# Kernel optimization log

Hardware: AMD Instinct MI355X
Metric: run time of the kernel (lower is better)

## Reference

```python
import jax, jax.numpy as jnp
import numpy as np

D_MODEL = 768
NUM_HEADS = 12
SEQ_LEN = 4096
BATCH = 1


def setup_inputs() -> dict:
    key = jax.random.key(0)
    k1, k2, k3, k4 = jax.random.split(key, 4)
    x = jax.random.normal(k1, (BATCH, SEQ_LEN, D_MODEL), dtype=jnp.float32)
    # nn.Linear(d_model, 3*d_model, bias=False): store as [d_model, 3*d_model] so h = x @ w_qkv
    w_qkv = jax.random.normal(k2, (D_MODEL, 3 * D_MODEL), dtype=jnp.float32) * (1.0 / np.sqrt(D_MODEL))
    w_proj = jax.random.normal(k3, (D_MODEL, D_MODEL), dtype=jnp.float32) * (1.0 / np.sqrt(D_MODEL))
    b_proj = jax.random.normal(k4, (D_MODEL,), dtype=jnp.float32) * 0.01
    return {"x": x, "w_qkv": w_qkv, "w_proj": w_proj, "b_proj": b_proj}


def reference(x, w_qkv, w_proj, b_proj):
    n, t, c = x.shape
    H = NUM_HEADS
    dh = c // H
    # fused QKV projection: [n, t, 3c] -> per head contiguous [q|k|v] chunks of dh
    h = (x @ w_qkv).reshape(n, t, H, 3, dh)
    q = h[..., 0, :]  # [n, t, H, dh]
    k = h[..., 1, :]
    v = h[..., 2, :]
    scale = 1.0 / np.sqrt(dh)
    # full TxT score matrix, as in the hand-rolled torch module
    scores = jnp.einsum('nqhd,nkhd->nhqk', q, k) * scale  # [n, H, t, t]
    causal = jnp.tril(jnp.ones((t, t), dtype=bool))  # tril buffer
    scores = jnp.where(causal, scores, jnp.finfo(scores.dtype).min)
    att = jax.nn.softmax(scores, axis=-1)
    out = jnp.einsum('nhqk,nkhd->nqhd', att, v).reshape(n, t, c)
    return out @ w_proj + b_proj
```

## Files before the change

### kernel.cpp

```cpp
#include <hip/hip_runtime.h>

#define T_SEQ 4096
#define DM    768
#define NH    12
#define DH    64
#define NC    2304

using half8  = __attribute__((ext_vector_type(8))) _Float16;
using half4v = __attribute__((ext_vector_type(4))) _Float16;
using f32x4  = __attribute__((ext_vector_type(4))) float;
using f32x16 = __attribute__((ext_vector_type(16))) float;
typedef unsigned int u32;

union H8 { half8 v; u32 u[4]; };

__device__ __forceinline__ u32 pkrtz_u32(float a, float b) {
    return __builtin_bit_cast(u32, __builtin_amdgcn_cvt_pkrtz(a, b));
}
__device__ __forceinline__ float asf(u32 x) { return __builtin_bit_cast(float, x); }
__device__ __forceinline__ u32 asu(float x) { return __builtin_bit_cast(u32, x); }

__device__ __forceinline__ void async_copy16(void* lds, const void* g) {
    __builtin_amdgcn_global_load_lds(
        (const __attribute__((address_space(1))) u32*)g,
        (__attribute__((address_space(3))) u32*)lds, 16, 0, 0);
}

__global__ __launch_bounds__(256)
void convert_x_kernel(const float* __restrict__ x, _Float16* __restrict__ xh) {
    const size_t i = ((size_t)blockIdx.x * 256 + threadIdx.x) * 8;
    float4 a = *(const float4*)(x + i);
    float4 b = *(const float4*)(x + i + 4);
    half8 o = { (_Float16)a.x, (_Float16)a.y, (_Float16)a.z, (_Float16)a.w,
                (_Float16)b.x, (_Float16)b.y, (_Float16)b.z, (_Float16)b.w };
    *(half8*)(xh + i) = o;
}

__global__ __launch_bounds__(256)
void transpose_convert_kernel(const float* __restrict__ src,
                              _Float16* __restrict__ dst, int R, int C) {
    __shared__ _Float16 tile[64][72];
    const int tid = threadIdx.x;
    const int tc0 = blockIdx.x * 64;
    const int tr0 = blockIdx.y * 64;
    const int r = tid >> 2, c4 = (tid & 3) * 16;
    const float* sp = src + (size_t)(tr0 + r) * C + tc0 + c4;
    #pragma unroll
    for (int j = 0; j < 16; j += 4) {
        float4 t4 = *(const float4*)(sp + j);
        tile[r][c4 + j + 0] = (_Float16)t4.x;
        tile[r][c4 + j + 1] = (_Float16)t4.y;
        tile[r][c4 + j + 2] = (_Float16)t4.z;
        tile[r][c4 + j + 3] = (_Float16)t4.w;
    }
    __syncthreads();
    const int c = tid >> 2, r4 = (tid & 3) * 16;
    half8 o0, o1;
    #pragma unroll
    for (int j = 0; j < 8; ++j) o0[j] = tile[r4 + j][c];
    #pragma unroll
    for (int j = 0; j < 8; ++j) o1[j] = tile[r4 + 8 + j][c];
    _Float16* dp = dst + (size_t)(tc0 + c) * R + tr0 + r4;
    *(half8*)(dp) = o0;
    *(half8*)(dp + 8) = o1;
}

__global__ __launch_bounds__(256, 2)
void qkv_mfma_kernel(const _Float16* __restrict__ A,
                     const _Float16* __restrict__ Bt,
                     _Float16* __restrict__ q, _Float16* __restrict__ k,
                     _Float16* __restrict__ v) {
    __shared__ _Float16 Alds[128 * 64];
    __shared__ _Float16 Blds[128 * 64];
    const int tid  = threadIdx.x;
    const int lane = tid & 63;
    const int w    = tid >> 6;
    const int wr = w >> 1, wc = w & 1;
    const int lrow = lane >> 4, lcol = lane & 15;

    const int bid  = blockIdx.x;
    const int virt = (bid & 7) * 72 + (bid >> 3);
    const int cbn  = virt % 18, rbn = virt / 18;

    const _Float16* Ag = A  + (size_t)rbn * 128 * DM;
    const _Float16* Bg = Bt + (size_t)cbn * 128 * DM;

    int srow[4], scol[4];
    #pragma unroll
    for (int i = 0; i < 4; ++i) {
        const int idx = i * 256 + tid;
        srow[i] = idx >> 3;
        scol[i] = ((idx & 7) ^ (srow[i] & 7)) * 8;
    }

    f32x4 acc[4][4];
    #pragma unroll
    for (int mf = 0; mf < 4; ++mf)
        #pragma unroll
        for (int nf = 0; nf < 4; ++nf) acc[mf][nf] = (f32x4){0.f, 0.f, 0.f, 0.f};

    for (int kt = 0; kt < DM / 64; ++kt) {
        const int k0 = kt * 64;
        __syncthreads();
        #pragma unroll
        for (int i = 0; i < 4; ++i) {
            async_copy16((char*)Alds + (i * 256 + w * 64) * 16,
                         Ag + (size_t)srow[i] * DM + k0 + scol[i]);
            async_copy16((char*)Blds + (i * 256 + w * 64) * 16,
                         Bg + (size_t)srow[i] * DM + k0 + scol[i]);
        }
        __syncthreads();
        #pragma unroll
        for (int kh = 0; kh < 2; ++kh) {
            half8 af[4], bf[4];
            const int ag = kh * 4 + lrow;
            #pragma unroll
            for (int f = 0; f < 4; ++f) {
                const int ar = wr * 64 + f * 16 + lcol;
                af[f] = *(const half8*)((const char*)Alds +
                          ar * 128 + ((ag ^ (ar & 7)) << 4));
                const int br = wc * 64 + f * 16 + lcol;
                bf[f] = *(const half8*)((const char*)Blds +
                          br * 128 + ((ag ^ (br & 7)) << 4));
            }
            #pragma unroll
            for (int mf = 0; mf < 4; ++mf)
                #pragma unroll
                for (int nf = 0; nf < 4; ++nf)
                    acc[mf][nf] = __builtin_amdgcn_mfma_f32_16x16x32_f16(
                        af[mf], bf[nf], acc[mf][nf], 0, 0, 0);
        }
    }

    #pragma unroll
    for (int nf = 0; nf < 4; ++nf) {
        const int n = cbn * 128 + wc * 64 + nf * 16 + lcol;
        const int head  = n / 192;
        const int which = (n >> 6) % 3;
        const int d = n & 63;
        _Float16* dst = (which == 0) ? q : (which == 1) ? k : v;
        const float sc = (which == 0) ? 0.18033688011112042f : 1.0f;
        dst += (size_t)head * T_SEQ * DH + d;
        #pragma unroll
        for (int mf = 0; mf < 4; ++mf) {
            const int t0 = rbn * 128 + wr * 64 + mf * 16 + lrow * 4;
            #pragma unroll
            for (int r = 0; r < 4; ++r)
                dst[(size_t)(t0 + r) * DH] = (_Float16)(acc[mf][nf][r] * sc);
        }
    }
}

__global__ __launch_bounds__(256, 2)
void proj_mfma_kernel(const _Float16* __restrict__ A,
                      const _Float16* __restrict__ Bt,
                      const float* __restrict__ bias, float* __restrict__ out) {
    __shared__ _Float16 Alds[128 * 64];
    __shared__ _Float16 Blds[128 * 64];
    const int tid  = threadIdx.x;
    const int lane = tid & 63;
    const int w    = tid >> 6;
    const int wr = w >> 1, wc = w & 1;
    const int lrow = lane >> 4, lcol = lane & 15;

    const int bid  = blockIdx.x;
    const int virt = (bid & 7) * 24 + (bid >> 3);
    const int cbn  = virt % 6, rbn = virt / 6;

    const _Float16* Ag = A  + (size_t)rbn * 128 * DM;
    const _Float16* Bg = Bt + (size_t)cbn * 128 * DM;

    int srow[4], scol[4];
    #pragma unroll
    for (int i = 0; i < 4; ++i) {
        const int idx = i * 256 + tid;
        srow[i] = idx >> 3;
        scol[i] = ((idx & 7) ^ (srow[i] & 7)) * 8;
    }

    f32x4 acc[4][4];
    #pragma unroll
    for (int mf = 0; mf < 4; ++mf)
        #pragma unroll
        for (int nf = 0; nf < 4; ++nf) acc[mf][nf] = (f32x4){0.f, 0.f, 0.f, 0.f};

    for (int kt = 0; kt < DM / 64; ++kt) {
        const int k0 = kt * 64;
        __syncthreads();
        #pragma unroll
        for (int i = 0; i < 4; ++i) {
            async_copy16((char*)Alds + (i * 256 + w * 64) * 16,
                         Ag + (size_t)srow[i] * DM + k0 + scol[i]);
            async_copy16((char*)Blds + (i * 256 + w * 64) * 16,
                         Bg + (size_t)srow[i] * DM + k0 + scol[i]);
        }
        __syncthreads();
        #pragma unroll
        for (int kh = 0; kh < 2; ++kh) {
            half8 af[4], bf[4];
            const int ag = kh * 4 + lrow;
            #pragma unroll
            for (int f = 0; f < 4; ++f) {
                const int ar = wr * 64 + f * 16 + lcol;
                af[f] = *(const half8*)((const char*)Alds +
                          ar * 128 + ((ag ^ (ar & 7)) << 4));
                const int br = wc * 64 + f * 16 + lcol;
                bf[f] = *(const half8*)((const char*)Blds +
                          br * 128 + ((ag ^ (br & 7)) << 4));
            }
            #pragma unroll
            for (int mf = 0; mf < 4; ++mf)
                #pragma unroll
                for (int nf = 0; nf < 4; ++nf)
                    acc[mf][nf] = __builtin_amdgcn_mfma_f32_16x16x32_f16(
                        af[mf], bf[nf], acc[mf][nf], 0, 0, 0);
        }
    }

    #pragma unroll
    for (int nf = 0; nf < 4; ++nf) {
        const int n = cbn * 128 + wc * 64 + nf * 16 + lcol;
        const float b = bias[n];
        #pragma unroll
        for (int mf = 0; mf < 4; ++mf) {
            const int t0 = rbn * 128 + wr * 64 + mf * 16 + lrow * 4;
            #pragma unroll
            for (int r = 0; r < 4; ++r)
                out[(size_t)(t0 + r) * DM + n] = acc[mf][nf][r] + b;
        }
    }
}

__global__ __launch_bounds__(256)
void vt_kernel(const _Float16* __restrict__ v, _Float16* __restrict__ vt) {
    __shared__ _Float16 tile[64][65];
    const int tid = threadIdx.x;
    const int tb = blockIdx.x, h = blockIdx.y;
    const int r = tid >> 2, c0 = (tid & 3) * 16;
    const _Float16* src = v + ((size_t)h * T_SEQ + tb * 64 + r) * 64 + c0;
    half8 a0 = *(const half8*)(src);
    half8 a1 = *(const half8*)(src + 8);
    #pragma unroll
    for (int j = 0; j < 8; ++j) tile[r][c0 + j] = a0[j];
    #pragma unroll
    for (int j = 0; j < 8; ++j) tile[r][c0 + 8 + j] = a1[j];
    __syncthreads();
    const int d = tid >> 2, t0 = (tid & 3) * 16;
    half8 o0, o1;
    #pragma unroll
    for (int j = 0; j < 8; ++j) o0[j] = tile[t0 + j][d];
    #pragma unroll
    for (int j = 0; j < 8; ++j) o1[j] = tile[t0 + 8 + j][d];
    _Float16* dst = vt + ((size_t)h * 64 + d) * T_SEQ + tb * 64 + t0;
    *(half8*)(dst) = o0;
    *(half8*)(dst + 8) = o1;
}

__global__ __launch_bounds__(256)
void attn_tile_kernel(const _Float16* __restrict__ qg,
                      const _Float16* __restrict__ kg,
                      const _Float16* __restrict__ vtg,
                      _Float16* __restrict__ pO,
                      float* __restrict__ pml) {
    __shared__ _Float16 Kl[2][4096];
    __shared__ _Float16 Vl[2][4096];

    const int tid  = threadIdx.x;
    const int lane = tid & 63;
    const int w    = tid >> 6;
    const int l31  = lane & 31;
    const int hi   = lane >> 5;

    const int b = blockIdx.x;
    const int h = b % NH;
    const int i = 79 - b / NH;
    int j, seg;
    if (i < 8)       { j = i;                  seg = 0; }
    else if (i < 24) { const int t = i - 8;    j = 8  + (t >> 1); seg = t & 1; }
    else if (i < 48) { const int t = i - 24;   j = 16 + t / 3;    seg = t % 3; }
    else             { const int t = i - 48;   j = 24 + (t >> 2); seg = t & 3; }

    const int cw      = 4 * j + w;
    const int q       = cw * 32 + l31;
    const int niter_w = 2 * j + 1 + (w >> 1);
    const int tS      = seg * 16;
    const int tEndBlk = min(tS + 16, 2 * j + 2);
    const int tEndW   = min(tS + 16, niter_w);

    const _Float16* Qh = qg  + ((size_t)h * T_SEQ + q) * DH;
    const _Float16* Kh = kg  + (size_t)h * T_SEQ * DH;
    const _Float16* Vh = vtg + (size_t)h * DH * T_SEQ;

    half8 qf[4];
    #pragma unroll
    for (int ks = 0; ks < 4; ++ks)
        qf[ks] = *(const half8*)(Qh + ks * 16 + hi * 8);

    f32x16 o0v = {}, o1v = {};
    float l = 0.f;

    const int g0 = tid, g1 = tid + 256;
    const int r0 = g0 >> 3, s0 = ((g0 & 7) ^ (r0 & 7)) * 8;
    const int r1 = g1 >> 3, s1 = ((g1 & 7) ^ (r1 & 7)) * 8;

    auto stage = [&](int p, int kvb) {
        async_copy16((char*)Kl[p] + g0 * 16, Kh + (size_t)(kvb + r0) * DH + s0);
        async_copy16((char*)Kl[p] + g1 * 16, Kh + (size_t)(kvb + r1) * DH + s1);
        async_copy16((char*)Vl[p] + g0 * 16, Vh + (size_t)r0 * T_SEQ + kvb + s0);
        async_copy16((char*)Vl[p] + g1 * 16, Vh + (size_t)r1 * T_SEQ + kvb + s1);
    };

    stage(0, tS * 64);
    for (int it = tS; it < tEndBlk; ++it) {
        const int p = (it - tS) & 1;
        __syncthreads();
        if (it + 1 < tEndBlk) stage(p ^ 1, (it + 1) * 64);
        if (it >= tEndW) continue;

        const int kvb = it * 64;
        const char* Kb = (const char*)Kl[p];
        const char* Vb = (const char*)Vl[p];
        const int sw7 = l31 & 7;

        half8 kfA[4], kfB[4];
        #pragma unroll
        for (int ks = 0; ks < 4; ++ks) {
            const int gsl = (ks * 2 + hi) ^ sw7;
            kfA[ks] = *(const half8*)(Kb + l31 * 128 + (gsl << 4));
            kfB[ks] = *(const half8*)(Kb + (32 + l31) * 128 + (gsl << 4));
        }
        half8 vf[2][2][2];
        #pragma unroll
        for (int t = 0; t < 2; ++t)
            #pragma unroll
            for (int dt = 0; dt < 2; ++dt)
                #pragma unroll
                for (int ks2 = 0; ks2 < 2; ++ks2) {
                    const int gsl = (t * 4 + ks2 * 2 + hi) ^ sw7;
                    vf[t][dt][ks2] = *(const half8*)(Vb +
                        (dt * 32 + l31) * 128 + (gsl << 4));
                }

        f32x16 sA, sB;
        #pragma unroll
        for (int r = 0; r < 16; ++r) { sA[r] = -8.0f; sB[r] = -8.0f; }
        __builtin_amdgcn_s_setprio(1);
        #pragma unroll
        for (int ks = 0; ks < 4; ++ks) {
            sA = __builtin_amdgcn_mfma_f32_32x32x16_f16(kfA[ks], qf[ks], sA, 0, 0, 0);
            sB = __builtin_amdgcn_mfma_f32_32x32x16_f16(kfB[ks], qf[ks], sB, 0, 0, 0);
        }
        __builtin_amdgcn_s_setprio(0);

        if (it == niter_w - 1) {
            #pragma unroll
            for (int r = 0; r < 16; ++r) {
                const int off = (r & 3) + 8 * (r >> 2) + 4 * hi;
                if (kvb + off > q)      sA[r] = -1e30f;
                if (kvb + 32 + off > q) sB[r] = -1e30f;
            }
        }

        #pragma unroll
        for (int r = 0; r < 16; ++r) sA[r] = __builtin_amdgcn_exp2f(sA[r]);
        #pragma unroll
        for (int r = 0; r < 16; ++r) sB[r] = __builtin_amdgcn_exp2f(sB[r]);
        float s8[8];
        #pragma unroll
        for (int r = 0; r < 8; ++r)
            s8[r] = (sA[r] + sA[r + 8]) + (sB[r] + sB[r + 8]);
        float rsum = ((s8[0] + s8[4]) + (s8[1] + s8[5])) +
                     ((s8[2] + s8[6]) + (s8[3] + s8[7]));
        {
            auto r = __builtin_amdgcn_permlane32_swap(asu(rsum), asu(rsum), false, false);
            rsum = asf(r[0]) + asf(r[1]);
        }
        l += rsum;

        H8 pfA[2], pfB[2];
        #pragma unroll
        for (int ks2 = 0; ks2 < 2; ++ks2) {
            {
                const u32 a0 = pkrtz_u32(sA[8*ks2+0], sA[8*ks2+1]);
                const u32 a1 = pkrtz_u32(sA[8*ks2+2], sA[8*ks2+3]);
                const u32 b0 = pkrtz_u32(sA[8*ks2+4], sA[8*ks2+5]);
                const u32 b1 = pkrtz_u32(sA[8*ks2+6], sA[8*ks2+7]);
                auto r0v = __builtin_amdgcn_permlane32_swap(a0, b0, false, false);
                auto r1v = __builtin_amdgcn_permlane32_swap(a1, b1, false, false);
                pfA[ks2].u[0] = r0v[0];
                pfA[ks2].u[1] = r1v[0];
                pfA[ks2].u[2] = r0v[1];
                pfA[ks2].u[3] = r1v[1];
            }
            {
                const u32 a0 = pkrtz_u32(sB[8*ks2+0], sB[8*ks2+1]);
                const u32 a1 = pkrtz_u32(sB[8*ks2+2], sB[8*ks2+3]);
                const u32 b0 = pkrtz_u32(sB[8*ks2+4], sB[8*ks2+5]);
                const u32 b1 = pkrtz_u32(sB[8*ks2+6], sB[8*ks2+7]);
                auto r0v = __builtin_amdgcn_permlane32_swap(a0, b0, false, false);
                auto r1v = __builtin_amdgcn_permlane32_swap(a1, b1, false, false);
                pfB[ks2].u[0] = r0v[0];
                pfB[ks2].u[1] = r1v[0];
                pfB[ks2].u[2] = r0v[1];
                pfB[ks2].u[3] = r1v[1];
            }
        }

        __builtin_amdgcn_s_setprio(1);
        #pragma unroll
        for (int ks2 = 0; ks2 < 2; ++ks2) {
            o0v = __builtin_amdgcn_mfma_f32_32x32x16_f16(vf[0][0][ks2], pfA[ks2].v, o0v, 0, 0, 0);
            o1v = __builtin_amdgcn_mfma_f32_32x32x16_f16(vf[0][1][ks2], pfA[ks2].v, o1v, 0, 0, 0);
            o0v = __builtin_amdgcn_mfma_f32_32x32x16_f16(vf[1][0][ks2], pfB[ks2].v, o0v, 0, 0, 0);
            o1v = __builtin_amdgcn_mfma_f32_32x32x16_f16(vf[1][1][ks2], pfB[ks2].v, o1v, 0, 0, 0);
        }
        __builtin_amdgcn_s_setprio(0);
    }

    const int hc = h * 128 + cw;
    const float inv = (l > 0.f) ? 1.0f / l : 0.f;
    _Float16* op = pO + ((size_t)(seg * 1536 + hc) * 32 + l31) * 64 + 4 * hi;
    #pragma unroll
    for (int g = 0; g < 4; ++g) {
        half4v w0 = { (_Float16)(o0v[4*g+0] * inv), (_Float16)(o0v[4*g+1] * inv),
                      (_Float16)(o0v[4*g+2] * inv), (_Float16)(o0v[4*g+3] * inv) };
        half4v w1 = { (_Float16)(o1v[4*g+0] * inv), (_Float16)(o1v[4*g+1] * inv),
                      (_Float16)(o1v[4*g+2] * inv), (_Float16)(o1v[4*g+3] * inv) };
        *(half4v*)(op + 8 * g)      = w0;
        *(half4v*)(op + 32 + 8 * g) = w1;
    }
    if (hi == 0) {
        float* mp = pml + ((size_t)(seg * 1536 + hc) * 32 + l31) * 2;
        mp[0] = 0.0f;
        mp[1] = l;
    }
}

__global__ __launch_bounds__(256)
void attn_combine_kernel(const _Float16* __restrict__ pO,
                         const float* __restrict__ pml,
                         _Float16* __restrict__ att) {
    const int row = blockIdx.x * 256 + threadIdx.x;
    const int q5 = row & 31;
    const int hc = row >> 5;
    const int c  = hc & 127;
    const int h  = hc >> 7;
    const int nseg = 1 + (c >= 32) + (c >= 64) + (c >= 96);

    float mm[4], ll[4];
    float M = -1e30f;
    #pragma unroll
    for (int s = 0; s < 4; ++s) {
        const bool on = s < nseg;
        const float* mp = pml + ((size_t)(s * 1536 + hc) * 32 + q5) * 2;
        mm[s] = on ? mp[0] : -1e30f;
        ll[s] = on ? mp[1] : 0.f;
        M = fmaxf(M, mm[s]);
    }
    float wgt[4];
    float L = 0.f;
    #pragma unroll
    for (int s = 0; s < 4; ++s) {
        wgt[s] = ll[s] * __builtin_amdgcn_exp2f(mm[s] - M);
        L += wgt[s];
    }
    const float invL = 1.0f / L;
    #pragma unroll
    for (int s = 0; s < 4; ++s) wgt[s] *= invL;

    float acc[64];
    #pragma unroll
    for (int d = 0; d < 64; ++d) acc[d] = 0.f;
    #pragma unroll
    for (int s = 0; s < 4; ++s) {
        if (s >= nseg) break;
        const _Float16* src = pO + ((size_t)(s * 1536 + hc) * 32 + q5) * 64;
        const float wsc = wgt[s];
        #pragma unroll
        for (int g = 0; g < 8; ++g) {
            half8 v = *(const half8*)(src + g * 8);
            #pragma unroll
            for (int jj = 0; jj < 8; ++jj)
                acc[g * 8 + jj] += wsc * (float)v[jj];
        }
    }
    _Float16* dst = att + (size_t)(c * 32 + q5) * DM + h * DH;
    #pragma unroll
    for (int g = 0; g < 8; ++g) {
        half8 o;
        #pragma unroll
        for (int jj = 0; jj < 8; ++jj) o[jj] = (_Float16)acc[g * 8 + jj];
        *(half8*)(dst + g * 8) = o;
    }
}

extern "C" void kernel_launch(void* const* d_in, const int* in_sizes, int n_in,
                              void* d_out, int out_size, void* d_ws, size_t ws_size,
                              hipStream_t stream) {
    const float* x      = (const float*)d_in[0];
    const float* w_qkv  = (const float*)d_in[1];
    const float* w_proj = (const float*)d_in[2];
    const float* b_proj = (const float*)d_in[3];
    float* out = (float*)d_out;

    _Float16* wsb = (_Float16*)d_ws;
    const size_t XS = (size_t)T_SEQ * DM;
    const size_t HS = (size_t)NH * T_SEQ * DH;
    _Float16* xh     = wsb;
    _Float16* wqkvT  = xh + XS;
    _Float16* wprojT = wqkvT + (size_t)NC * DM;
    _Float16* q      = wprojT + (size_t)DM * DM;
    _Float16* k      = q + HS;
    _Float16* v      = k + HS;
    _Float16* vt     = v + HS;
    _Float16* att    = vt + HS;
    _Float16* pO     = att + XS;
    float*    pml    = (float*)(pO + (size_t)4 * 1536 * 32 * 64);

    convert_x_kernel<<<dim3(1536), 256, 0, stream>>>(x, xh);
    transpose_convert_kernel<<<dim3(36, 12), 256, 0, stream>>>(w_qkv, wqkvT, DM, NC);
    transpose_convert_kernel<<<dim3(12, 12), 256, 0, stream>>>(w_proj, wprojT, DM, DM);
    qkv_mfma_kernel<<<dim3(576), 256, 0, stream>>>(xh, wqkvT, q, k, v);
    vt_kernel<<<dim3(64, NH), 256, 0, stream>>>(v, vt);
    attn_tile_kernel<<<dim3(960), 256, 0, stream>>>(q, k, vt, pO, pml);
    attn_combine_kernel<<<dim3(192), 256, 0, stream>>>(pO, pml, att);
    proj_mfma_kernel<<<dim3(192), 256, 0, stream>>>(att, wprojT, b_proj, out);
}
```

Before: 120.1 us.

## Fuse V transpose into QKV GEMM and process two query chunks per attention block

The QKV GEMM epilogue now writes V directly in transposed layout, so the separate vt_kernel launch and its extra read and write of V are gone. The attention tile kernel now has each warp handle two 32-row query chunks against the same staged K/V tile. This halves the grid and reuses each LDS tile and its fragment loads for twice the queries. The combine kernel drops the unused max-based rescaling, since partial maxima are always zero. The cost is more accumulator registers per thread under a launch bound of 2 blocks, and fewer blocks to balance the causal triangle across CUs.

```diff
diff --git a/kernel.cpp b/kernel.cpp
--- a/kernel.cpp
+++ b/kernel.cpp
@@ -69,7 +69,7 @@
 void qkv_mfma_kernel(const _Float16* __restrict__ A,
                      const _Float16* __restrict__ Bt,
                      _Float16* __restrict__ q, _Float16* __restrict__ k,
-                     _Float16* __restrict__ v) {
+                     _Float16* __restrict__ vt) {
     __shared__ _Float16 Alds[128 * 64];
     __shared__ _Float16 Blds[128 * 64];
     const int tid  = threadIdx.x;
@@ -138,15 +138,26 @@
         const int head  = n / 192;
         const int which = (n >> 6) % 3;
         const int d = n & 63;
-        _Float16* dst = (which == 0) ? q : (which == 1) ? k : v;
-        const float sc = (which == 0) ? 0.18033688011112042f : 1.0f;
-        dst += (size_t)head * T_SEQ * DH + d;
-        #pragma unroll
-        for (int mf = 0; mf < 4; ++mf) {
-            const int t0 = rbn * 128 + wr * 64 + mf * 16 + lrow * 4;
-            #pragma unroll
-            for (int r = 0; r < 4; ++r)
-                dst[(size_t)(t0 + r) * DH] = (_Float16)(acc[mf][nf][r] * sc);
+        if (which == 2) {
+            _Float16* dv = vt + ((size_t)head * DH + d) * T_SEQ;
+            #pragma unroll
+            for (int mf = 0; mf < 4; ++mf) {
+                const int t0 = rbn * 128 + wr * 64 + mf * 16 + lrow * 4;
+                half4v o = { (_Float16)acc[mf][nf][0], (_Float16)acc[mf][nf][1],
+                             (_Float16)acc[mf][nf][2], (_Float16)acc[mf][nf][3] };
+                *(half4v*)(dv + t0) = o;
+            }
+        } else {
+            _Float16* dst = (which == 0) ? q : k;
+            const float sc = (which == 0) ? 0.18033688011112042f : 1.0f;
+            dst += (size_t)head * T_SEQ * DH + d;
+            #pragma unroll
+            for (int mf = 0; mf < 4; ++mf) {
+                const int t0 = rbn * 128 + wr * 64 + mf * 16 + lrow * 4;
+                #pragma unroll
+                for (int r = 0; r < 4; ++r)
+                    dst[(size_t)(t0 + r) * DH] = (_Float16)(acc[mf][nf][r] * sc);
+            }
         }
     }
 }
@@ -231,32 +242,7 @@
     }
 }
 
-__global__ __launch_bounds__(256)
-void vt_kernel(const _Float16* __restrict__ v, _Float16* __restrict__ vt) {
-    __shared__ _Float16 tile[64][65];
-    const int tid = threadIdx.x;
-    const int tb = blockIdx.x, h = blockIdx.y;
-    const int r = tid >> 2, c0 = (tid & 3) * 16;
-    const _Float16* src = v + ((size_t)h * T_SEQ + tb * 64 + r) * 64 + c0;
-    half8 a0 = *(const half8*)(src);
-    half8 a1 = *(const half8*)(src + 8);
-    #pragma unroll
-    for (int j = 0; j < 8; ++j) tile[r][c0 + j] = a0[j];
-    #pragma unroll
-    for (int j = 0; j < 8; ++j) tile[r][c0 + 8 + j] = a1[j];
-    __syncthreads();
-    const int d = tid >> 2, t0 = (tid & 3) * 16;
-    half8 o0, o1;
-    #pragma unroll
-    for (int j = 0; j < 8; ++j) o0[j] = tile[t0 + j][d];
-    #pragma unroll
-    for (int j = 0; j < 8; ++j) o1[j] = tile[t0 + 8 + j][d];
-    _Float16* dst = vt + ((size_t)h * 64 + d) * T_SEQ + tb * 64 + t0;
-    *(half8*)(dst) = o0;
-    *(half8*)(dst + 8) = o1;
-}
-
-__global__ __launch_bounds__(256)
+__global__ __launch_bounds__(256, 2)
 void attn_tile_kernel(const _Float16* __restrict__ qg,
                       const _Float16* __restrict__ kg,
                       const _Float16* __restrict__ vtg,
@@ -273,31 +259,41 @@
 
     const int b = blockIdx.x;
     const int h = b % NH;
-    const int i = 79 - b / NH;
+    const int i = 39 - b / NH;
     int j, seg;
-    if (i < 8)       { j = i;                  seg = 0; }
-    else if (i < 24) { const int t = i - 8;    j = 8  + (t >> 1); seg = t & 1; }
-    else if (i < 48) { const int t = i - 24;   j = 16 + t / 3;    seg = t % 3; }
-    else             { const int t = i - 48;   j = 24 + (t >> 2); seg = t & 3; }
-
-    const int cw      = 4 * j + w;
-    const int q       = cw * 32 + l31;
-    const int niter_w = 2 * j + 1 + (w >> 1);
+    if (i < 4)       { j = i;                 seg = 0; }
+    else if (i < 12) { const int t = i - 4;   j = 4  + (t >> 1); seg = t & 1; }
+    else if (i < 24) { const int t = i - 12;  j = 8  + t / 3;    seg = t % 3; }
+    else             { const int t = i - 24;  j = 12 + (t >> 2); seg = t & 3; }
+
+    const int c0 = 8 * j + w;
+    const int c1 = 8 * j + 4 + w;
+    const int q0 = c0 * 32 + l31;
+    const int q1 = c1 * 32 + l31;
+    const int niter0 = c0 / 2 + 1;
+    const int niter1 = c1 / 2 + 1;
     const int tS      = seg * 16;
-    const int tEndBlk = min(tS + 16, 2 * j + 2);
-    const int tEndW   = min(tS + 16, niter_w);
-
-    const _Float16* Qh = qg  + ((size_t)h * T_SEQ + q) * DH;
+    const int tEndBlk = min(tS + 16, 4 * j + 4);
+    const int tEnd0   = min(tS + 16, niter0);
+    const int tEnd1   = min(tS + 16, niter1);
+
     const _Float16* Kh = kg  + (size_t)h * T_SEQ * DH;
     const _Float16* Vh = vtg + (size_t)h * DH * T_SEQ;
 
-    half8 qf[4];
-    #pragma unroll
-    for (int ks = 0; ks < 4; ++ks)
-        qf[ks] = *(const half8*)(Qh + ks * 16 + hi * 8);
-
-    f32x16 o0v = {}, o1v = {};
-    float l = 0.f;
+    half8 qf0[4], qf1[4];
+    {
+        const _Float16* Q0 = qg + ((size_t)h * T_SEQ + q0) * DH + hi * 8;
+        const _Float16* Q1 = qg + ((size_t)h * T_SEQ + q1) * DH + hi * 8;
+        #pragma unroll
+        for (int ks = 0; ks < 4; ++ks) {
+            qf0[ks] = *(const half8*)(Q0 + ks * 16);
+            qf1[ks] = *(const half8*)(Q1 + ks * 16);
+        }
+    }
+
+    f32x16 oA0 = {}, oA1 = {};
+    f32x16 oB0 = {}, oB1 = {};
+    float l0 = 0.f, l1 = 0.f;
 
     const int g0 = tid, g1 = tid + 256;
     const int r0 = g0 >> 3, s0 = ((g0 & 7) ^ (r0 & 7)) * 8;
@@ -315,7 +311,7 @@
         const int p = (it - tS) & 1;
         __syncthreads();
         if (it + 1 < tEndBlk) stage(p ^ 1, (it + 1) * 64);
-        if (it >= tEndW) continue;
+        if (it >= tEnd1) continue;
 
         const int kvb = it * 64;
         const char* Kb = (const char*)Kl[p];
@@ -341,99 +337,109 @@
                         (dt * 32 + l31) * 128 + (gsl << 4));
                 }
 
-        f32x16 sA, sB;
-        #pragma unroll
-        for (int r = 0; r < 16; ++r) { sA[r] = -8.0f; sB[r] = -8.0f; }
-        __builtin_amdgcn_s_setprio(1);
-        #pragma unroll
-        for (int ks = 0; ks < 4; ++ks) {
-            sA = __builtin_amdgcn_mfma_f32_32x32x16_f16(kfA[ks], qf[ks], sA, 0, 0, 0);
-            sB = __builtin_amdgcn_mfma_f32_32x32x16_f16(kfB[ks], qf[ks], sB, 0, 0, 0);
-        }
-        __builtin_amdgcn_s_setprio(0);
-
-        if (it == niter_w - 1) {
-            #pragma unroll
-            for (int r = 0; r < 16; ++r) {
-                const int off = (r & 3) + 8 * (r >> 2) + 4 * hi;
-                if (kvb + off > q)      sA[r] = -1e30f;
-                if (kvb + 32 + off > q) sB[r] = -1e30f;
-            }
-        }
-
-        #pragma unroll
-        for (int r = 0; r < 16; ++r) sA[r] = __builtin_amdgcn_exp2f(sA[r]);
-        #pragma unroll
-        for (int r = 0; r < 16; ++r) sB[r] = __builtin_amdgcn_exp2f(sB[r]);
-        float s8[8];
-        #pragma unroll
-        for (int r = 0; r < 8; ++r)
-            s8[r] = (sA[r] + sA[r + 8]) + (sB[r] + sB[r + 8]);
-        float rsum = ((s8[0] + s8[4]) + (s8[1] + s8[5])) +
-                     ((s8[2] + s8[6]) + (s8[3] + s8[7]));
-        {
-            auto r = __builtin_amdgcn_permlane32_swap(asu(rsum), asu(rsum), false, false);
-            rsum = asf(r[0]) + asf(r[1]);
-        }
-        l += rsum;
-
-        H8 pfA[2], pfB[2];
-        #pragma unroll
-        for (int ks2 = 0; ks2 < 2; ++ks2) {
+        auto run_stream = [&](const half8* qf, f32x16& o0v, f32x16& o1v,
+                              float& lsum, int qrow, int niter) {
+            f32x16 sA, sB;
+            #pragma unroll
+            for (int r = 0; r < 16; ++r) { sA[r] = -8.0f; sB[r] = -8.0f; }
+            __builtin_amdgcn_s_setprio(1);
+            #pragma unroll
+            for (int ks = 0; ks < 4; ++ks) {
+                sA = __builtin_amdgcn_mfma_f32_32x32x16_f16(kfA[ks], qf[ks], sA, 0, 0, 0);
+                sB = __builtin_amdgcn_mfma_f32_32x32x16_f16(kfB[ks], qf[ks], sB, 0, 0, 0);
+            }
+            __builtin_amdgcn_s_setprio(0);
+
+            if (it == niter - 1) {
+                #pragma unroll
+                for (int r = 0; r < 16; ++r) {
+                    const int off = (r & 3) + 8 * (r >> 2) + 4 * hi;
+                    if (kvb + off > qrow)      sA[r] = -1e30f;
+                    if (kvb + 32 + off > qrow) sB[r] = -1e30f;
+                }
+            }
+
+            #pragma unroll
+            for (int r = 0; r < 16; ++r) sA[r] = __builtin_amdgcn_exp2f(sA[r]);
+            #pragma unroll
+            for (int r = 0; r < 16; ++r) sB[r] = __builtin_amdgcn_exp2f(sB[r]);
+            float s8[8];
+            #pragma unroll
+            for (int r = 0; r < 8; ++r)
+                s8[r] = (sA[r] + sA[r + 8]) + (sB[r] + sB[r + 8]);
+            float rsum = ((s8[0] + s8[4]) + (s8[1] + s8[5])) +
+                         ((s8[2] + s8[6]) + (s8[3] + s8[7]));
             {
-                const u32 a0 = pkrtz_u32(sA[8*ks2+0], sA[8*ks2+1]);
-                const u32 a1 = pkrtz_u32(sA[8*ks2+2], sA[8*ks2+3]);
-                const u32 b0 = pkrtz_u32(sA[8*ks2+4], sA[8*ks2+5]);
-                const u32 b1 = pkrtz_u32(sA[8*ks2+6], sA[8*ks2+7]);
-                auto r0v = __builtin_amdgcn_permlane32_swap(a0, b0, false, false);
-                auto r1v = __builtin_amdgcn_permlane32_swap(a1, b1, false, false);
-                pfA[ks2].u[0] = r0v[0];
-                pfA[ks2].u[1] = r1v[0];
-                pfA[ks2].u[2] = r0v[1];
-                pfA[ks2].u[3] = r1v[1];
-            }
-            {
-                const u32 a0 = pkrtz_u32(sB[8*ks2+0], sB[8*ks2+1]);
-                const u32 a1 = pkrtz_u32(sB[8*ks2+2], sB[8*ks2+3]);
-                const u32 b0 = pkrtz_u32(sB[8*ks2+4], sB[8*ks2+5]);
-                const u32 b1 = pkrtz_u32(sB[8*ks2+6], sB[8*ks2+7]);
-                auto r0v = __builtin_amdgcn_permlane32_swap(a0, b0, false, false);
-                auto r1v = __builtin_amdgcn_permlane32_swap(a1, b1, false, false);
-                pfB[ks2].u[0] = r0v[0];
-                pfB[ks2].u[1] = r1v[0];
-                pfB[ks2].u[2] = r0v[1];
-                pfB[ks2].u[3] = r1v[1];
-            }
-        }
-
-        __builtin_amdgcn_s_setprio(1);
-        #pragma unroll
-        for (int ks2 = 0; ks2 < 2; ++ks2) {
-            o0v = __builtin_amdgcn_mfma_f32_32x32x16_f16(vf[0][0][ks2], pfA[ks2].v, o0v, 0, 0, 0);
-            o1v = __builtin_amdgcn_mfma_f32_32x32x16_f16(vf[0][1][ks2], pfA[ks2].v, o1v, 0, 0, 0);
-            o0v = __builtin_amdgcn_mfma_f32_32x32x16_f16(vf[1][0][ks2], pfB[ks2].v, o0v, 0, 0, 0);
-            o1v = __builtin_amdgcn_mfma_f32_32x32x16_f16(vf[1][1][ks2], pfB[ks2].v, o1v, 0, 0, 0);
-        }
-        __builtin_amdgcn_s_setprio(0);
-    }
-
-    const int hc = h * 128 + cw;
-    const float inv = (l > 0.f) ? 1.0f / l : 0.f;
-    _Float16* op = pO + ((size_t)(seg * 1536 + hc) * 32 + l31) * 64 + 4 * hi;
-    #pragma unroll
-    for (int g = 0; g < 4; ++g) {
-        half4v w0 = { (_Float16)(o0v[4*g+0] * inv), (_Float16)(o0v[4*g+1] * inv),
-                      (_Float16)(o0v[4*g+2] * inv), (_Float16)(o0v[4*g+3] * inv) };
-        half4v w1 = { (_Float16)(o1v[4*g+0] * inv), (_Float16)(o1v[4*g+1] * inv),
-                      (_Float16)(o1v[4*g+2] * inv), (_Float16)(o1v[4*g+3] * inv) };
-        *(half4v*)(op + 8 * g)      = w0;
-        *(half4v*)(op + 32 + 8 * g) = w1;
-    }
-    if (hi == 0) {
-        float* mp = pml + ((size_t)(seg * 1536 + hc) * 32 + l31) * 2;
-        mp[0] = 0.0f;
-        mp[1] = l;
-    }
+                auto rr = __builtin_amdgcn_permlane32_swap(asu(rsum), asu(rsum), false, false);
+                rsum = asf(rr[0]) + asf(rr[1]);
+            }
+            lsum += rsum;
+
+            H8 pfA[2], pfB[2];
+            #pragma unroll
+            for (int ks2 = 0; ks2 < 2; ++ks2) {
+                {
+                    const u32 a0 = pkrtz_u32(sA[8*ks2+0], sA[8*ks2+1]);
+                    const u32 a1 = pkrtz_u32(sA[8*ks2+2], sA[8*ks2+3]);
+                    const u32 b0 = pkrtz_u32(sA[8*ks2+4], sA[8*ks2+5]);
+                    const u32 b1 = pkrtz_u32(sA[8*ks2+6], sA[8*ks2+7]);
+                    auto r0v = __builtin_amdgcn_permlane32_swap(a0, b0, false, false);
+                    auto r1v = __builtin_amdgcn_permlane32_swap(a1, b1, false, false);
+                    pfA[ks2].u[0] = r0v[0];
+                    pfA[ks2].u[1] = r1v[0];
+                    pfA[ks2].u[2] = r0v[1];
+                    pfA[ks2].u[3] = r1v[1];
+                }
+                {
+                    const u32 a0 = pkrtz_u32(sB[8*ks2+0], sB[8*ks2+1]);
+                    const u32 a1 = pkrtz_u32(sB[8*ks2+2], sB[8*ks2+3]);
+                    const u32 b0 = pkrtz_u32(sB[8*ks2+4], sB[8*ks2+5]);
+                    const u32 b1 = pkrtz_u32(sB[8*ks2+6], sB[8*ks2+7]);
+                    auto r0v = __builtin_amdgcn_permlane32_swap(a0, b0, false, false);
+                    auto r1v = __builtin_amdgcn_permlane32_swap(a1, b1, false, false);
+                    pfB[ks2].u[0] = r0v[0];
+                    pfB[ks2].u[1] = r1v[0];
+                    pfB[ks2].u[2] = r0v[1];
+                    pfB[ks2].u[3] = r1v[1];
+                }
+            }
+
+            __builtin_amdgcn_s_setprio(1);
+            #pragma unroll
+            for (int ks2 = 0; ks2 < 2; ++ks2) {
+                o0v = __builtin_amdgcn_mfma_f32_32x32x16_f16(vf[0][0][ks2], pfA[ks2].v, o0v, 0, 0, 0);
+                o1v = __builtin_amdgcn_mfma_f32_32x32x16_f16(vf[0][1][ks2], pfA[ks2].v, o1v, 0, 0, 0);
+                o0v = __builtin_amdgcn_mfma_f32_32x32x16_f16(vf[1][0][ks2], pfB[ks2].v, o0v, 0, 0, 0);
+                o1v = __builtin_amdgcn_mfma_f32_32x32x16_f16(vf[1][1][ks2], pfB[ks2].v, o1v, 0, 0, 0);
+            }
+            __builtin_amdgcn_s_setprio(0);
+        };
+
+        if (it < tEnd0) run_stream(qf0, oA0, oA1, l0, q0, niter0);
+        run_stream(qf1, oB0, oB1, l1, q1, niter1);
+    }
+
+    auto write_partial = [&](int c, const f32x16& o0v, const f32x16& o1v, float l) {
+        const int hc = h * 128 + c;
+        const float inv = (l > 0.f) ? 1.0f / l : 0.f;
+        _Float16* op = pO + ((size_t)(seg * 1536 + hc) * 32 + l31) * 64 + 4 * hi;
+        #pragma unroll
+        for (int g = 0; g < 4; ++g) {
+            half4v w0 = { (_Float16)(o0v[4*g+0] * inv), (_Float16)(o0v[4*g+1] * inv),
+                          (_Float16)(o0v[4*g+2] * inv), (_Float16)(o0v[4*g+3] * inv) };
+            half4v w1 = { (_Float16)(o1v[4*g+0] * inv), (_Float16)(o1v[4*g+1] * inv),
+                          (_Float16)(o1v[4*g+2] * inv), (_Float16)(o1v[4*g+3] * inv) };
+            *(half4v*)(op + 8 * g)      = w0;
+            *(half4v*)(op + 32 + 8 * g) = w1;
+        }
+        if (hi == 0) {
+            float* mp = pml + ((size_t)(seg * 1536 + hc) * 32 + l31) * 2;
+            mp[0] = 0.0f;
+            mp[1] = l;
+        }
+    };
+    write_partial(c0, oA0, oA1, l0);
+    write_partial(c1, oB0, oB1, l1);
 }
 
 __global__ __launch_bounds__(256)
@@ -445,28 +451,18 @@
     const int hc = row >> 5;
     const int c  = hc & 127;
     const int h  = hc >> 7;
-    const int nseg = 1 + (c >= 32) + (c >= 64) + (c >= 96);
-
-    float mm[4], ll[4];
-    float M = -1e30f;
+    const int nseg = c / 32 + 1;
+
+    float ll[4];
+    float L = 0.f;
     #pragma unroll
     for (int s = 0; s < 4; ++s) {
         const bool on = s < nseg;
         const float* mp = pml + ((size_t)(s * 1536 + hc) * 32 + q5) * 2;
-        mm[s] = on ? mp[0] : -1e30f;
         ll[s] = on ? mp[1] : 0.f;
-        M = fmaxf(M, mm[s]);
-    }
-    float wgt[4];
-    float L = 0.f;
-    #pragma unroll
-    for (int s = 0; s < 4; ++s) {
-        wgt[s] = ll[s] * __builtin_amdgcn_exp2f(mm[s] - M);
-        L += wgt[s];
+        L += ll[s];
     }
     const float invL = 1.0f / L;
-    #pragma unroll
-    for (int s = 0; s < 4; ++s) wgt[s] *= invL;
 
     float acc[64];
     #pragma unroll
@@ -475,7 +471,7 @@
     for (int s = 0; s < 4; ++s) {
         if (s >= nseg) break;
         const _Float16* src = pO + ((size_t)(s * 1536 + hc) * 32 + q5) * 64;
-        const float wsc = wgt[s];
+        const float wsc = ll[s] * invL;
         #pragma unroll
         for (int g = 0; g < 8; ++g) {
             half8 v = *(const half8*)(src + g * 8);
@@ -511,8 +507,7 @@
     _Float16* wprojT = wqkvT + (size_t)NC * DM;
     _Float16* q      = wprojT + (size_t)DM * DM;
     _Float16* k      = q + HS;
-    _Float16* v      = k + HS;
-    _Float16* vt     = v + HS;
+    _Float16* vt     = k + HS;
     _Float16* att    = vt + HS;
     _Float16* pO     = att + XS;
     float*    pml    = (float*)(pO + (size_t)4 * 1536 * 32 * 64);
@@ -520,9 +515,8 @@
     convert_x_kernel<<<dim3(1536), 256, 0, stream>>>(x, xh);
     transpose_convert_kernel<<<dim3(36, 12), 256, 0, stream>>>(w_qkv, wqkvT, DM, NC);
     transpose_convert_kernel<<<dim3(12, 12), 256, 0, stream>>>(w_proj, wprojT, DM, DM);
-    qkv_mfma_kernel<<<dim3(576), 256, 0, stream>>>(xh, wqkvT, q, k, v);
-    vt_kernel<<<dim3(64, NH), 256, 0, stream>>>(v, vt);
-    attn_tile_kernel<<<dim3(960), 256, 0, stream>>>(q, k, vt, pO, pml);
+    qkv_mfma_kernel<<<dim3(576), 256, 0, stream>>>(xh, wqkvT, q, k, vt);
+    attn_tile_kernel<<<dim3(480), 256, 0, stream>>>(q, k, vt, pO, pml);
     attn_combine_kernel<<<dim3(192), 256, 0, stream>>>(pO, pml, att);
     proj_mfma_kernel<<<dim3(192), 256, 0, stream>>>(att, wprojT, b_proj, out);
 }
```

Result: faster. 104.9 us (-12.6%).
